# Performance work log

Hardware: AMD Instinct MI355X
Metric: run time of the kernel (lower is better)

The kernel has to match this reference:

```python
import jax, jax.numpy as jnp
import numpy as np

N_NODES = 50000
N_EDGES = 800000
IN_CH = 128
OUT_CH = 128
TIME_DIM = 64


def setup_inputs() -> dict:
    key = jax.random.key(0)
    ks = jax.random.split(key, 7)
    x = jax.random.normal(ks[0], (N_NODES, IN_CH), dtype=jnp.float32)
    edge_index = jax.random.randint(ks[1], (2, N_EDGES), 0, N_NODES, dtype=jnp.int64)
    edge_t = jax.random.uniform(ks[2], (N_EDGES,), dtype=jnp.float32)
    # parameters
    freqs = jax.random.normal(ks[3], (TIME_DIM // 2,), dtype=jnp.float32)
    fan = IN_CH + TIME_DIM
    lim = float(np.sqrt(1.0 / fan))
    lin_w = jax.random.uniform(ks[4], (OUT_CH, fan), minval=-lim, maxval=lim, dtype=jnp.float32)
    lin_b = jax.random.uniform(ks[5], (OUT_CH,), minval=-lim, maxval=lim, dtype=jnp.float32)
    glim = float(np.sqrt(6.0 / (1 + OUT_CH)))
    attn = jax.random.uniform(ks[6], (1, OUT_CH), minval=-glim, maxval=glim, dtype=jnp.float32)
    return {"x": x, "edge_index": edge_index, "edge_t": edge_t,
            "freqs": freqs, "lin_w": lin_w, "lin_b": lin_b, "attn": attn}


def reference(x, edge_index, edge_t, freqs, lin_w, lin_b, attn):
    src, dst = edge_index[0], edge_index[1]
    n_nodes = x.shape[0]
    # time encoding: [E, time_dim]
    ang = edge_t[:, None] * freqs * (2.0 * jnp.pi)
    edge_attr = jnp.concatenate([jnp.sin(ang), jnp.cos(ang)], axis=-1)
    # gather source features and project: h = tanh(Linear(cat(x_j, te)))
    msg = jnp.concatenate([x[src], edge_attr], axis=-1)        # [E, in+time]
    h = jnp.tanh(msg @ lin_w.T + lin_b)                        # [E, out]
    # segment softmax over destination nodes
    alpha = (h * attn).sum(axis=-1)                            # [E]
    seg_max = jax.ops.segment_max(alpha, dst, num_segments=n_nodes)
    ex = jnp.exp(alpha - seg_max[dst])
    denom = jax.ops.segment_sum(ex, dst, num_segments=n_nodes)
    w = ex / (denom[dst] + 1e-16)
    # scatter-add aggregation
    out = jax.ops.segment_sum(h * w[:, None], dst, num_segments=n_nodes)
    return out
```

## Files before the change

kernel.cpp:

```cpp
#include <hip/hip_runtime.h>
#include <hip/hip_bf16.h>
#include <math.h>

#define IN_CHN 128
#define OUT_CHN 128
#define KD 192
#define TM 64
#define HXP 136

typedef __bf16 bf16x8 __attribute__((ext_vector_type(8)));
typedef float f32x4 __attribute__((ext_vector_type(4)));

static __device__ __forceinline__ unsigned short f2b(float f) {
    return __builtin_bit_cast(unsigned short, (__bf16)f);
}
static __device__ __forceinline__ float b2f(unsigned short b) {
    return __uint_as_float(((unsigned int)b) << 16);
}
static __device__ __forceinline__ float fast_tanh(float x) {
    float e = __expf(2.0f * x);
    return 1.0f - 2.0f * __builtin_amdgcn_rcpf(e + 1.0f);
}

#define GLL16(gsrc, ldst) \
    __builtin_amdgcn_global_load_lds( \
        (const __attribute__((address_space(1))) unsigned int*)(gsrc), \
        (__attribute__((address_space(3))) unsigned int*)(ldst), 16, 0, 0)

#define LDS_BARRIER() do { \
    asm volatile("s_waitcnt lgkmcnt(0)" ::: "memory"); \
    __builtin_amdgcn_s_barrier(); \
    __builtin_amdgcn_sched_barrier(0); \
} while (0)


__global__ __launch_bounds__(256) void cvt_cnt(const float* __restrict__ x,
    unsigned short* __restrict__ xb, const int* __restrict__ ei,
    int* __restrict__ deg, int* __restrict__ side_node,
    long long n8, int E, int nb)
{
    long long i = (long long)blockIdx.x * 256 + threadIdx.x;
    if (i < n8) {
        const float4* src = (const float4*)(x + i * 8);
        float4 v0 = src[0], v1 = src[1];
        ushort4 p0 = { f2b(v0.x), f2b(v0.y), f2b(v0.z), f2b(v0.w) };
        ushort4 p1 = { f2b(v1.x), f2b(v1.y), f2b(v1.z), f2b(v1.w) };
        *(ushort4*)(xb + i * 8)     = p0;
        *(ushort4*)(xb + i * 8 + 4) = p1;
    }
    int t = (int)i;
    if (t < E) atomicAdd(&deg[ei[E + t]], 1);
    if (t < nb) side_node[t] = -1;
}


static __device__ __forceinline__ int wave_incl_scan(int v, int lane) {
    #pragma unroll
    for (int off = 1; off < 64; off <<= 1) {
        int t = __shfl_up(v, off);
        if (lane >= off) v += t;
    }
    return v;
}

__global__ __launch_bounds__(256) void scan_local(const int* __restrict__ deg,
    int* __restrict__ offs, int* __restrict__ partial, int Nn)
{
    __shared__ int wsum[4];
    int tid = threadIdx.x, lane = tid & 63, wid = tid >> 6;
    int i = blockIdx.x * 256 + tid;
    int v = (i < Nn) ? deg[i] : 0;
    int incl = wave_incl_scan(v, lane);
    if (lane == 63) wsum[wid] = incl;
    __syncthreads();
    int wpre = 0;
    for (int w = 0; w < wid; ++w) wpre += wsum[w];
    if (i < Nn) offs[i] = wpre + incl - v;
    if (tid == 255) partial[blockIdx.x] = wpre + incl;
}

__global__ __launch_bounds__(256) void finalize2(int* __restrict__ offs,
    const int* __restrict__ partial, int* __restrict__ cursor,
    int Nn, int E, int nblk)
{
    __shared__ int wsum[4];
    int b = blockIdx.x, tid = threadIdx.x, lane = tid & 63, wid = tid >> 6;
    int v = (tid < b && tid < nblk) ? partial[tid] : 0;
    #pragma unroll
    for (int off = 32; off > 0; off >>= 1) v += __shfl_xor(v, off);
    if (lane == 0) wsum[wid] = v;
    __syncthreads();
    int bp = wsum[0] + wsum[1] + wsum[2] + wsum[3];
    int i = b * 256 + tid;
    if (i < Nn) {
        int o = offs[i] + bp;
        offs[i] = o; cursor[i] = o;
        if (i == Nn - 1) offs[Nn] = E;
    }
}

__global__ __launch_bounds__(256) void fill_perm(const int* __restrict__ ei,
    const float* __restrict__ et, int* __restrict__ cursor,
    uint2* __restrict__ mt, int E)
{
    int e = blockIdx.x * 256 + threadIdx.x;
    if (e < E) {
        int d = ei[E + e];
        int pos = atomicAdd(&cursor[d], 1);
        mt[pos] = make_uint2((unsigned)ei[e], __float_as_uint(et[e]));
    }
}


__device__ __forceinline__ void load_meta(const uint2* __restrict__ mt,
    int tile, int E, int rbase, int g, int trow, int sv[2], float& tsv)
{
    int e0 = tile * TM;
    #pragma unroll
    for (int i = 0; i < 2; ++i) {
        int e = e0 + rbase + i * 4 + g;
        sv[i] = (int)mt[e < E ? e : E - 1].x;
    }
    int el = e0 + trow;
    tsv = __uint_as_float(mt[el < E ? el : E - 1].y);
}

__global__ __launch_bounds__(512) void gemm_fused(
    const unsigned short* __restrict__ xb, const uint2* __restrict__ mt,
    const int* __restrict__ offs,
    const float* __restrict__ freqs, const float* __restrict__ lw,
    const float* __restrict__ lb, const float* __restrict__ attn,
    float* __restrict__ out, float* __restrict__ den_g,
    int* __restrict__ side_node, float* __restrict__ side_den,
    float* __restrict__ side_val,
    int E, int Nn, int n_tiles, int kq, int kr)
{
    __shared__ unsigned short xs[2][TM][128];
    __shared__ unsigned short te[2][TM * 64];
    __shared__ unsigned short hx[TM * HXP];
    __shared__ float exs[2][TM];

    const int b    = blockIdx.x;
    const int t0   = b * kq + min(b, kr);
    const int cnt  = kq + (b < kr ? 1 : 0);
    if (cnt <= 0 || t0 >= n_tiles) return;
    const int tend = min(t0 + cnt, n_tiles);
    const int be0  = t0 * TM;
    const int bend = min(tend * TM, E);

    const int tid  = threadIdx.x;
    const int lane = tid & 63;
    const int wv   = tid >> 6;
    const int c16  = lane & 15;
    const int g    = lane >> 4;
    const int wbase = wv * 16;
    const int rbase = wv * 8;
    const int trow  = tid >> 3;
    const int tpart = tid & 7;
    const int sub  = lane >> 4;
    const int chl  = lane & 15;

    bf16x8 Wf[6];
    #pragma unroll
    for (int kk = 0; kk < 6; ++kk) {
        const float* wp = lw + (size_t)(wbase + c16) * KD + kk * 32 + g * 8;
        float4 v0 = *(const float4*)wp;
        float4 v1 = *(const float4*)(wp + 4);
        bf16x8 bb;
        bb[0] = (__bf16)v0.x; bb[1] = (__bf16)v0.y; bb[2] = (__bf16)v0.z; bb[3] = (__bf16)v0.w;
        bb[4] = (__bf16)v1.x; bb[5] = (__bf16)v1.y; bb[6] = (__bf16)v1.z; bb[7] = (__bf16)v1.w;
        Wf[kk] = bb;
    }
    const f32x4 bias_v = *(const f32x4*)(lb   + wbase + g * 4);
    const f32x4 attn_v = *(const f32x4*)(attn + wbase + g * 4);

    const float coff = (tpart >= 4) ? 1.5707963267948966f : 0.0f;
    float frv[8];
    #pragma unroll
    for (int j = 0; j < 8; ++j) frv[j] = freqs[(tpart & 3) * 8 + j] * 6.283185307179586f;

    int n0;
    {
        int lo = 0, hi = Nn;
        while (lo + 1 < hi) {
            int mid = (lo + hi) >> 1;
            if (offs[mid] <= be0) lo = mid; else hi = mid;
        }
        n0 = lo;
    }
    int cur_node = n0 + ((wv - (n0 & 7)) & 7);
    float a[8];
    #pragma unroll
    for (int q = 0; q < 8; ++q) a[q] = 0.0f;
    float den = 0.0f;

    float ts_nxt;
    int sv_nxt[2];
    {
        int sv0[2]; float ts0;
        load_meta(mt, t0, E, rbase, g, trow, sv0, ts0);
        #pragma unroll
        for (int i = 0; i < 2; ++i) {
            const int rlo = (rbase + i * 4 + g) & 15;
            const unsigned short* gsrc = xb + (size_t)sv0[i] * IN_CHN + ((c16 ^ rlo) * 8);
            GLL16(gsrc, &xs[0][rbase + i * 4][0]);
        }
        float v[8];
        #pragma unroll
        for (int j = 0; j < 8; ++j)
            v[j] = __sinf(ts0 * frv[j] + coff);
        unsigned short* tr = &te[0][trow * 64];
        int slot = (tpart ^ (trow & 7)) * 8;
        *(ushort4*)(tr + slot)     = (ushort4){ f2b(v[0]), f2b(v[1]), f2b(v[2]), f2b(v[3]) };
        *(ushort4*)(tr + slot + 4) = (ushort4){ f2b(v[4]), f2b(v[5]), f2b(v[6]), f2b(v[7]) };
        if (tid < TM) exs[0][tid] = 0.0f;

        int t1 = t0 + 1;
        load_meta(mt, t1 < tend ? t1 : tend - 1, E, rbase, g, trow, sv_nxt, ts_nxt);
    }

    int cur = 0;
    for (int tile = t0; tile < tend; ++tile) {
        const int e0 = tile * TM;
        const int e1 = e0 + TM;

        {
            float v[8];
            #pragma unroll
            for (int j = 0; j < 8; ++j)
                v[j] = __sinf(ts_nxt * frv[j] + coff);
            unsigned short* tr = &te[cur ^ 1][trow * 64];
            int slot = (tpart ^ (trow & 7)) * 8;
            *(ushort4*)(tr + slot)     = (ushort4){ f2b(v[0]), f2b(v[1]), f2b(v[2]), f2b(v[3]) };
            *(ushort4*)(tr + slot + 4) = (ushort4){ f2b(v[4]), f2b(v[5]), f2b(v[6]), f2b(v[7]) };
        }
        int sv2[2]; float ts2;
        {
            int t2 = tile + 2;
            load_meta(mt, t2 < tend ? t2 : tend - 1, E, rbase, g, trow, sv2, ts2);
        }

        __syncthreads();

        if (tile + 1 < tend) {
            #pragma unroll
            for (int i = 0; i < 2; ++i) {
                const int rlo = (rbase + i * 4 + g) & 15;
                const unsigned short* gsrc = xb + (size_t)sv_nxt[i] * IN_CHN + ((c16 ^ rlo) * 8);
                GLL16(gsrc, &xs[cur ^ 1][rbase + i * 4][0]);
            }
        }
        if (tid < TM) exs[cur ^ 1][tid] = 0.0f;

        f32x4 acc[4];
        #pragma unroll
        for (int mi = 0; mi < 4; ++mi) acc[mi] = (f32x4){0.f, 0.f, 0.f, 0.f};

        __builtin_amdgcn_s_setprio(1);
        const unsigned short* xsc = &xs[cur][0][0];
        const unsigned short* tec = &te[cur][0];
        #pragma unroll
        for (int mi = 0; mi < 4; ++mi) {
            const int r = mi * 16 + c16;
            const unsigned short* xrow = xsc + r * 128;
            #pragma unroll
            for (int kk = 0; kk < 4; ++kk) {
                const int slot = ((kk << 2) + g) ^ c16;
                bf16x8 av = __builtin_bit_cast(bf16x8, *(const uint4*)(xrow + slot * 8));
                acc[mi] = __builtin_amdgcn_mfma_f32_16x16x32_bf16(Wf[kk], av, acc[mi], 0, 0, 0);
            }
            const unsigned short* trw = tec + r * 64;
            bf16x8 s8 = __builtin_bit_cast(bf16x8, *(const uint4*)(trw + ((g ^ (r & 7)) * 8)));
            bf16x8 c8 = __builtin_bit_cast(bf16x8, *(const uint4*)(trw + (((g + 4) ^ (r & 7)) * 8)));
            acc[mi] = __builtin_amdgcn_mfma_f32_16x16x32_bf16(Wf[4], s8, acc[mi], 0, 0, 0);
            acc[mi] = __builtin_amdgcn_mfma_f32_16x16x32_bf16(Wf[5], c8, acc[mi], 0, 0, 0);
        }
        __builtin_amdgcn_s_setprio(0);

        #pragma unroll
        for (int mi = 0; mi < 4; ++mi) {
            const int r = mi * 16 + c16;
            f32x4 z = acc[mi];
            float p = 0.0f;
            #pragma unroll
            for (int q = 0; q < 4; ++q) {
                float h = fast_tanh(z[q] + bias_v[q]);
                z[q] = h;
                p = fmaf(h, attn_v[q], p);
            }
            ushort4 pv = (ushort4){ f2b(z[0]), f2b(z[1]), f2b(z[2]), f2b(z[3]) };
            *(ushort4*)&hx[r * HXP + wbase + g * 4] = pv;
            p += __shfl_xor(p, 16);
            p += __shfl_xor(p, 32);
            if (g == 0) atomicAdd(&exs[cur][r], p);
        }

        LDS_BARRIER();

        while (cur_node < Nn) {
            int s  = offs[cur_node];
            if (s >= e1) break;
            int en = offs[cur_node + 1];
            int lo = s > e0 ? s : e0;
            int hi = en < e1 ? en : e1;
            for (int i = lo + sub; i < hi; i += 4) {
                int li = i - e0;
                float ex = __expf(exs[cur][li]);
                uint4 hv = *(const uint4*)&hx[li * HXP + chl * 8];
                den += ex;
                unsigned int hw[4] = { hv.x, hv.y, hv.z, hv.w };
                #pragma unroll
                for (int q = 0; q < 4; ++q) {
                    a[2*q]   = fmaf(ex, b2f((unsigned short)(hw[q] & 0xFFFFu)), a[2*q]);
                    a[2*q+1] = fmaf(ex, b2f((unsigned short)(hw[q] >> 16)),     a[2*q+1]);
                }
            }
            if (en <= e1) {
                #pragma unroll
                for (int q = 0; q < 8; ++q) {
                    a[q] += __shfl_xor(a[q], 16);
                    a[q] += __shfl_xor(a[q], 32);
                }
                float ds = den + __shfl_xor(den, 16);
                ds += __shfl_xor(ds, 32);
                if (sub == 0) {
                    float* op = out + (size_t)cur_node * OUT_CHN + chl * 8;
                    if (s >= be0) {
                        float rs = __builtin_amdgcn_rcpf(ds + 1e-16f);
                        *(float4*)op       = (float4){a[0]*rs, a[1]*rs, a[2]*rs, a[3]*rs};
                        *(float4*)(op + 4) = (float4){a[4]*rs, a[5]*rs, a[6]*rs, a[7]*rs};
                    } else {
                        *(float4*)op       = (float4){a[0], a[1], a[2], a[3]};
                        *(float4*)(op + 4) = (float4){a[4], a[5], a[6], a[7]};
                        if (chl == 0) den_g[cur_node] = ds;
                    }
                }
                #pragma unroll
                for (int q = 0; q < 8; ++q) a[q] = 0.0f;
                den = 0.0f;
                cur_node += 8;
            } else break;
        }

        ts_nxt = ts2;
        sv_nxt[0] = sv2[0]; sv_nxt[1] = sv2[1];
        cur ^= 1;
    }

    if (cur_node < Nn) {
        int s = offs[cur_node];
        if (s < bend && offs[cur_node + 1] > bend) {
            #pragma unroll
            for (int q = 0; q < 8; ++q) {
                a[q] += __shfl_xor(a[q], 16);
                a[q] += __shfl_xor(a[q], 32);
            }
            float ds = den + __shfl_xor(den, 16);
            ds += __shfl_xor(ds, 32);
            if (sub == 0) {
                float* sv = side_val + (size_t)b * OUT_CHN + chl * 8;
                *(float4*)sv       = (float4){a[0], a[1], a[2], a[3]};
                *(float4*)(sv + 4) = (float4){a[4], a[5], a[6], a[7]};
                if (chl == 0) {
                    side_den[b] = ds;
                    side_node[b] = cur_node;
                }
            }
        }
    }
}


__global__ __launch_bounds__(256) void fixup2(const int* __restrict__ side_node,
    const float* __restrict__ side_den, const float* __restrict__ side_val,
    const int* __restrict__ offs,
    float* __restrict__ out, const float* __restrict__ den_g, int nb, int Nn)
{
    long long gid = (long long)blockIdx.x * 256 + threadIdx.x;
    if (gid < (long long)nb * 64) {
        int w = (int)(gid >> 6);
        int lane = (int)(gid & 63);
        int node = side_node[w];
        if (node < 0) return;
        const float* sv = side_val + (size_t)w * OUT_CHN;
        float* op = out + (size_t)node * OUT_CHN;
        float rs = __builtin_amdgcn_rcpf(den_g[node] + side_den[w] + 1e-16f);
        float2 o = *(float2*)(op + lane * 2);
        float2 s = *(const float2*)(sv + lane * 2);
        o.x = (o.x + s.x) * rs;
        o.y = (o.y + s.y) * rs;
        *(float2*)(op + lane * 2) = o;
    } else {
        int n = (int)(gid - (long long)nb * 64);
        if (n >= Nn) return;
        if (offs[n + 1] == offs[n]) {
            float* op = out + (size_t)n * OUT_CHN;
            for (int c = 0; c < OUT_CHN; c += 4)
                *(float4*)(op + c) = (float4){0, 0, 0, 0};
        }
    }
}


extern "C" void kernel_launch(void* const* d_in, const int* in_sizes, int n_in,
                              void* d_out, int out_size, void* d_ws, size_t ws_size,
                              hipStream_t stream) {
    const float* x     = (const float*)d_in[0];
    const int*   ei    = (const int*)d_in[1];
    const float* et    = (const float*)d_in[2];
    const float* freqs = (const float*)d_in[3];
    const float* lw    = (const float*)d_in[4];
    const float* lb    = (const float*)d_in[5];
    const float* attn  = (const float*)d_in[6];
    float* out = (float*)d_out;

    const int E  = in_sizes[2];
    const int Nn = in_sizes[0] / IN_CHN;
    const int NB = 512;

    char* ws = (char*)d_ws;
    uint2* mt      = (uint2*)ws;         size_t off = (size_t)E * sizeof(uint2);
    unsigned short* xb = (unsigned short*)(ws + off); off += (size_t)Nn * IN_CHN * sizeof(unsigned short);
    float* den_g   = (float*)(ws + off); off += (size_t)Nn * sizeof(float);
    int*   deg     = (int*)(ws + off);   off += (size_t)Nn * sizeof(int);
    int*   offs    = (int*)(ws + off);   off += (size_t)(Nn + 1) * sizeof(int);
    int*   cursor  = (int*)(ws + off);   off += (size_t)Nn * sizeof(int);
    int*   partial = (int*)(ws + off);   off += 1024 * sizeof(int);
    int*   side_node = (int*)(ws + off); off += 1024 * sizeof(int);
    float* side_den  = (float*)(ws + off); off += 1024 * sizeof(float);
    float* side_val  = (float*)(ws + off);

    const int nblk = (Nn + 255) / 256;
    const int eblk = (E + 255) / 256;

    hipMemsetAsync(deg, 0, (size_t)Nn * sizeof(int), stream);

    long long n8 = (long long)Nn * IN_CHN / 8;
    long long cgrid = n8 > (long long)E ? n8 : (long long)E;
    cvt_cnt<<<(unsigned)((cgrid + 255) / 256), 256, 0, stream>>>(
        x, xb, ei, deg, side_node, n8, E, NB);

    scan_local<<<nblk, 256, 0, stream>>>(deg, offs, partial, Nn);
    finalize2<<<nblk, 256, 0, stream>>>(offs, partial, cursor, Nn, E, nblk);
    fill_perm<<<eblk, 256, 0, stream>>>(ei, et, cursor, mt, E);

    const int n_tiles = (E + TM - 1) / TM;
    const int kq = n_tiles / NB, kr = n_tiles % NB;
    gemm_fused<<<NB, 512, 0, stream>>>(xb, mt, offs, freqs, lw, lb, attn,
                                       out, den_g, side_node, side_den, side_val,
                                       E, Nn, n_tiles, kq, kr);

    long long fthreads = (long long)NB * 64 + Nn;
    fixup2<<<(unsigned)((fthreads + 255) / 256), 256, 0, stream>>>(
        side_node, side_den, side_val, offs, out, den_g, NB, Nn);
}
```

Measured before the change: 230.1 us.

## Retile MFMA GEMM so each wave computes 32 edges by 32 channels

```diff
diff --git a/kernel.cpp b/kernel.cpp
--- a/kernel.cpp
+++ b/kernel.cpp
@@ -153,26 +153,35 @@
     const int wv   = tid >> 6;
     const int c16  = lane & 15;
     const int g    = lane >> 4;
-    const int wbase = wv * 16;
+    const int we   = wv & 1;
+    const int wc   = wv >> 1;
+    const int cbase = wc * 32;
+    const int ebase = we * 32;
     const int rbase = wv * 8;
     const int trow  = tid >> 3;
     const int tpart = tid & 7;
     const int sub  = lane >> 4;
     const int chl  = lane & 15;
 
-    bf16x8 Wf[6];
-    #pragma unroll
-    for (int kk = 0; kk < 6; ++kk) {
-        const float* wp = lw + (size_t)(wbase + c16) * KD + kk * 32 + g * 8;
-        float4 v0 = *(const float4*)wp;
-        float4 v1 = *(const float4*)(wp + 4);
-        bf16x8 bb;
-        bb[0] = (__bf16)v0.x; bb[1] = (__bf16)v0.y; bb[2] = (__bf16)v0.z; bb[3] = (__bf16)v0.w;
-        bb[4] = (__bf16)v1.x; bb[5] = (__bf16)v1.y; bb[6] = (__bf16)v1.z; bb[7] = (__bf16)v1.w;
-        Wf[kk] = bb;
-    }
-    const f32x4 bias_v = *(const f32x4*)(lb   + wbase + g * 4);
-    const f32x4 attn_v = *(const f32x4*)(attn + wbase + g * 4);
+    bf16x8 Wf[6][2];
+    #pragma unroll
+    for (int kk = 0; kk < 6; ++kk)
+        #pragma unroll
+        for (int nf = 0; nf < 2; ++nf) {
+            const float* wp = lw + (size_t)(cbase + nf * 16 + c16) * KD + kk * 32 + g * 8;
+            float4 v0 = *(const float4*)wp;
+            float4 v1 = *(const float4*)(wp + 4);
+            bf16x8 bb;
+            bb[0] = (__bf16)v0.x; bb[1] = (__bf16)v0.y; bb[2] = (__bf16)v0.z; bb[3] = (__bf16)v0.w;
+            bb[4] = (__bf16)v1.x; bb[5] = (__bf16)v1.y; bb[6] = (__bf16)v1.z; bb[7] = (__bf16)v1.w;
+            Wf[kk][nf] = bb;
+        }
+    f32x4 bias_v[2], attn_v[2];
+    #pragma unroll
+    for (int nf = 0; nf < 2; ++nf) {
+        bias_v[nf] = *(const f32x4*)(lb   + cbase + nf * 16 + g * 4);
+        attn_v[nf] = *(const f32x4*)(attn + cbase + nf * 16 + g * 4);
+    }
 
     const float coff = (tpart >= 4) ? 1.5707963267948966f : 0.0f;
     float frv[8];
@@ -252,44 +261,56 @@
         }
         if (tid < TM) exs[cur ^ 1][tid] = 0.0f;
 
-        f32x4 acc[4];
-        #pragma unroll
-        for (int mi = 0; mi < 4; ++mi) acc[mi] = (f32x4){0.f, 0.f, 0.f, 0.f};
+        f32x4 acc[2][2];
+        #pragma unroll
+        for (int mi = 0; mi < 2; ++mi) {
+            acc[mi][0] = (f32x4){0.f, 0.f, 0.f, 0.f};
+            acc[mi][1] = (f32x4){0.f, 0.f, 0.f, 0.f};
+        }
 
         __builtin_amdgcn_s_setprio(1);
         const unsigned short* xsc = &xs[cur][0][0];
         const unsigned short* tec = &te[cur][0];
         #pragma unroll
-        for (int mi = 0; mi < 4; ++mi) {
-            const int r = mi * 16 + c16;
+        for (int mi = 0; mi < 2; ++mi) {
+            const int r = ebase + mi * 16 + c16;
             const unsigned short* xrow = xsc + r * 128;
             #pragma unroll
             for (int kk = 0; kk < 4; ++kk) {
                 const int slot = ((kk << 2) + g) ^ c16;
                 bf16x8 av = __builtin_bit_cast(bf16x8, *(const uint4*)(xrow + slot * 8));
-                acc[mi] = __builtin_amdgcn_mfma_f32_16x16x32_bf16(Wf[kk], av, acc[mi], 0, 0, 0);
+                acc[mi][0] = __builtin_amdgcn_mfma_f32_16x16x32_bf16(Wf[kk][0], av, acc[mi][0], 0, 0, 0);
+                acc[mi][1] = __builtin_amdgcn_mfma_f32_16x16x32_bf16(Wf[kk][1], av, acc[mi][1], 0, 0, 0);
             }
             const unsigned short* trw = tec + r * 64;
             bf16x8 s8 = __builtin_bit_cast(bf16x8, *(const uint4*)(trw + ((g ^ (r & 7)) * 8)));
             bf16x8 c8 = __builtin_bit_cast(bf16x8, *(const uint4*)(trw + (((g + 4) ^ (r & 7)) * 8)));
-            acc[mi] = __builtin_amdgcn_mfma_f32_16x16x32_bf16(Wf[4], s8, acc[mi], 0, 0, 0);
-            acc[mi] = __builtin_amdgcn_mfma_f32_16x16x32_bf16(Wf[5], c8, acc[mi], 0, 0, 0);
+            acc[mi][0] = __builtin_amdgcn_mfma_f32_16x16x32_bf16(Wf[4][0], s8, acc[mi][0], 0, 0, 0);
+            acc[mi][1] = __builtin_amdgcn_mfma_f32_16x16x32_bf16(Wf[4][1], s8, acc[mi][1], 0, 0, 0);
+            acc[mi][0] = __builtin_amdgcn_mfma_f32_16x16x32_bf16(Wf[5][0], c8, acc[mi][0], 0, 0, 0);
+            acc[mi][1] = __builtin_amdgcn_mfma_f32_16x16x32_bf16(Wf[5][1], c8, acc[mi][1], 0, 0, 0);
         }
         __builtin_amdgcn_s_setprio(0);
 
         #pragma unroll
-        for (int mi = 0; mi < 4; ++mi) {
-            const int r = mi * 16 + c16;
-            f32x4 z = acc[mi];
+        for (int mi = 0; mi < 2; ++mi) {
+            const int r = ebase + mi * 16 + c16;
             float p = 0.0f;
+            ushort4 pv[2];
             #pragma unroll
-            for (int q = 0; q < 4; ++q) {
-                float h = fast_tanh(z[q] + bias_v[q]);
-                z[q] = h;
-                p = fmaf(h, attn_v[q], p);
-            }
-            ushort4 pv = (ushort4){ f2b(z[0]), f2b(z[1]), f2b(z[2]), f2b(z[3]) };
-            *(ushort4*)&hx[r * HXP + wbase + g * 4] = pv;
+            for (int nf = 0; nf < 2; ++nf) {
+                f32x4 z = acc[mi][nf];
+                #pragma unroll
+                for (int q = 0; q < 4; ++q) {
+                    float h = fast_tanh(z[q] + bias_v[nf][q]);
+                    z[q] = h;
+                    p = fmaf(h, attn_v[nf][q], p);
+                }
+                pv[nf] = (ushort4){ f2b(z[0]), f2b(z[1]), f2b(z[2]), f2b(z[3]) };
+            }
+            unsigned short* hp = &hx[r * HXP + cbase + g * 4];
+            *(ushort4*)hp        = pv[0];
+            *(ushort4*)(hp + 16) = pv[1];
             p += __shfl_xor(p, 16);
             p += __shfl_xor(p, 32);
             if (g == 0) atomicAdd(&exs[cur][r], p);
```

Measured after the change: 267.2 us. 16.1% more time.
